# Kernel optimization log

Hardware: AMD Instinct MI355X
Metric: run time of the kernel (lower is better)

The kernel has to match this reference:

```python
import jax, jax.numpy as jnp
import numpy as np

B, T, C, HS = 8, 2048, 1024, 128

def setup_inputs() -> dict:
    key = jax.random.key(0)
    kx, kq, kk, kv = jax.random.split(key, 4)
    x = jax.random.normal(kx, (B, T, C), dtype=jnp.float32)
    # torch Linear(C, HS, bias=False): y = x @ W^T with W [HS, C].
    # We store the transposed form [C, HS] and right-multiply (same math).
    scale = 1.0 / np.sqrt(C)  # torch default init scale-ish; exact init irrelevant for correctness
    Wq = jax.random.normal(kq, (C, HS), dtype=jnp.float32) * scale
    Wk = jax.random.normal(kk, (C, HS), dtype=jnp.float32) * scale
    Wv = jax.random.normal(kv, (C, HS), dtype=jnp.float32) * scale
    return {"x": x, "Wq": Wq, "Wk": Wk, "Wv": Wv}

def reference(x, Wq, Wk, Wv):
    Bx, Tx, Cx = x.shape
    q = x @ Wq  # [B, T, HS]
    k = x @ Wk
    v = x @ Wv
    # NOTE: original scales by C**-0.5 where C = n_embd (not head_size)
    wei = jnp.einsum('btd,bsd->bts', q, k) * (Cx ** -0.5)  # [B, T, T]
    causal = jnp.tril(jnp.ones((Tx, Tx), dtype=bool))
    wei = jnp.where(causal, wei, -jnp.inf)
    wei = jax.nn.softmax(wei, axis=-1)
    # dropout rate 0.0 (eval semantics) -> identity
    return jnp.einsum('bts,bsd->btd', wei, v)  # [B, T, HS]
```

## Files before the change

kernel.cpp:

```cpp
#include <hip/hip_runtime.h>
#include <hip/hip_bf16.h>
#include <stdint.h>

typedef float f32x4 __attribute__((ext_vector_type(4)));
typedef float f32x4v __attribute__((ext_vector_type(4)));
typedef short short8 __attribute__((ext_vector_type(8)));
typedef unsigned short u16;
typedef unsigned short u16x8 __attribute__((ext_vector_type(8)));
typedef unsigned short u16x4 __attribute__((ext_vector_type(4)));

#define MFMA16x16x32 __builtin_amdgcn_mfma_f32_16x16x32_bf16

__device__ __forceinline__ u16 f2bf(float f) {
    unsigned int u = __builtin_bit_cast(unsigned int, f);
    u += 0x7fffu + ((u >> 16) & 1u);
    return (u16)(u >> 16);
}

__device__ __forceinline__ void gload_lds16(const void* g, void* l) {
    __builtin_amdgcn_global_load_lds(
        (const __attribute__((address_space(1))) uint32_t*)g,
        (__attribute__((address_space(3))) uint32_t*)l, 16, 0, 0);
}

__device__ __forceinline__ void barrier_lgkm() {
    asm volatile("s_waitcnt lgkmcnt(0)\n\ts_barrier" ::: "memory");
}

__global__ void k_transpose_wf(const float* __restrict__ Wq, const float* __restrict__ Wk,
                               const float* __restrict__ Wv, u16* __restrict__ WTf) {
    int tid  = blockIdx.x * 256 + threadIdx.x;
    int f    = tid >> 6;
    int lane = tid & 63;
    int kt  = f / 48;
    int rem = f % 48;
    int ks  = rem / 24;
    int nc  = rem % 24;
    int col = nc * 16 + (lane & 15);
    int w   = col >> 7, n = col & 127;
    int k0  = kt * 64 + ks * 32 + (lane >> 4) * 8;
    const float* W = (w == 0) ? Wq : ((w == 1) ? Wk : Wv);
    u16x8 v;
#pragma unroll
    for (int j = 0; j < 8; ++j)
        v[j] = f2bf(W[(size_t)(k0 + j) * 128 + n]);
    *(u16x8*)(&WTf[(size_t)tid * 8]) = v;
}

__global__ __launch_bounds__(256) void k_qkv_gemm5(
    const float* __restrict__ x, const u16* __restrict__ WTf,
    u16* __restrict__ qb, u16* __restrict__ kb, u16* __restrict__ vT)
{
    __shared__ u16 la[32 * 64];
    const int tid  = threadIdx.x;
    const int lane = tid & 63, wid = tid >> 6;
    const int lrow = lane & 15, lk = lane >> 4;
    const int m0 = blockIdx.x * 32;

    const int arow = tid >> 3;
    const int aseg = tid & 7;
    const float* xsrc = x + (size_t)(m0 + arow) * 1024 + aseg * 8;

    f32x4 acc[2][6];
#pragma unroll
    for (int i = 0; i < 2; ++i)
#pragma unroll
        for (int j = 0; j < 6; ++j) acc[i][j] = (f32x4){0.f, 0.f, 0.f, 0.f};

    f32x4v pa0 = *(const f32x4v*)xsrc;
    f32x4v pa1 = *(const f32x4v*)(xsrc + 4);

    for (int kt = 0; kt < 16; ++kt) {
        barrier_lgkm();
        {
            u16x8 v;
            v[0] = f2bf(pa0[0]); v[1] = f2bf(pa0[1]); v[2] = f2bf(pa0[2]); v[3] = f2bf(pa0[3]);
            v[4] = f2bf(pa1[0]); v[5] = f2bf(pa1[1]); v[6] = f2bf(pa1[2]); v[7] = f2bf(pa1[3]);
            *(u16x8*)(&la[arow * 64 + ((aseg ^ (arow & 7)) << 3)]) = v;
        }
        if (kt + 1 < 16) {
            pa0 = *(const f32x4v*)(xsrc + (kt + 1) * 64);
            pa1 = *(const f32x4v*)(xsrc + (kt + 1) * 64 + 4);
        }
        short8 bf[2][6];
#pragma unroll
        for (int ks = 0; ks < 2; ++ks)
#pragma unroll
            for (int nf = 0; nf < 6; ++nf)
                bf[ks][nf] = *(const short8*)(
                    WTf + ((size_t)((kt * 2 + ks) * 24 + wid * 6 + nf) * 64 + lane) * 8);
        barrier_lgkm();
#pragma unroll
        for (int ks = 0; ks < 2; ++ks) {
            short8 af[2];
#pragma unroll
            for (int mf = 0; mf < 2; ++mf) {
                int row = mf * 16 + lrow;
                int blk = (ks * 4 + lk) ^ (row & 7);
                af[mf] = *(const short8*)(&la[row * 64 + (blk << 3)]);
            }
#pragma unroll
            for (int mf = 0; mf < 2; ++mf)
#pragma unroll
                for (int nf = 0; nf < 6; ++nf)
                    acc[mf][nf] = MFMA16x16x32(af[mf], bf[ks][nf], acc[mf][nf], 0, 0, 0);
        }
    }

#pragma unroll
    for (int nf = 0; nf < 6; ++nf) {
        const int gc   = wid * 96 + nf * 16 + lrow;
        const int wsel = gc >> 7;
        const int col  = gc & 127;
#pragma unroll
        for (int mf = 0; mf < 2; ++mf) {
            const int row0 = m0 + mf * 16 + lk * 4;
            if (wsel == 0) {
#pragma unroll
                for (int jj = 0; jj < 4; ++jj)
                    qb[(size_t)(row0 + jj) * 128 + col] = f2bf(acc[mf][nf][jj]);
            } else if (wsel == 1) {
#pragma unroll
                for (int jj = 0; jj < 4; ++jj)
                    kb[(size_t)(row0 + jj) * 128 + col] = f2bf(acc[mf][nf][jj]);
            } else {
                const int bb = row0 >> 11, t0 = row0 & 2047;
                u16x4 v;
#pragma unroll
                for (int jj = 0; jj < 4; ++jj) v[jj] = f2bf(acc[mf][nf][jj]);
                *(u16x4*)(&vT[((size_t)bb * 128 + col) * 2048 + t0]) = v;
            }
        }
    }
}

__global__ __launch_bounds__(256) void k_flash5(
    const u16* __restrict__ qb, const u16* __restrict__ kb, const u16* __restrict__ vT,
    float* __restrict__ po, float* __restrict__ pm, float* __restrict__ pl)
{
    __shared__ u16 k_lds[64 * 128];
    __shared__ u16 v_lds[128 * 64];
    __shared__ u16 p_lds[4 * 16 * 64];
    const int tid  = threadIdx.x;
    const int lane = tid & 63, wid = tid >> 6;
    const int lrow = lane & 15, lk = lane >> 4;
    const int bx = blockIdx.x;
    const int b  = bx & 7;
    const int qt = (bx >> 3) & 31;
    const int z  = bx >> 8;

    const int nt   = qt + 1;
    const int base = (nt + 3) >> 2;
    const int t0   = z * base;
    const int t1   = (t0 + base < nt) ? (t0 + base) : nt;

    float* poslab = po + (size_t)bx * (64 * 128);
    if (t0 >= nt) {
        f32x4 zero = (f32x4){0.f, 0.f, 0.f, 0.f};
#pragma unroll
        for (int i = 0; i < 8; ++i)
            *(f32x4*)(&poslab[(tid + i * 256) * 4]) = zero;
        if (tid < 64) { pm[(size_t)bx * 64 + tid] = -1e30f; pl[(size_t)bx * 64 + tid] = 0.f; }
        return;
    }

    const int qrow0 = qt * 64;
    short8 qf[4];
    {
        const u16* qp = qb + ((size_t)b * 2048 + qrow0 + wid * 16 + lrow) * 128;
#pragma unroll
        for (int ks = 0; ks < 4; ++ks) qf[ks] = *(const short8*)(qp + ks * 32 + lk * 8);
    }
    f32x4 of[8];
#pragma unroll
    for (int i = 0; i < 8; ++i) of[i] = (f32x4){0.f, 0.f, 0.f, 0.f};
    float mrun[4], lsum[4];
#pragma unroll
    for (int j = 0; j < 4; ++j) { mrun[j] = -1e30f; lsum[j] = 0.f; }

    const u16* kbase = kb + (size_t)b * 2048 * 128;
    const u16* vbase = vT + (size_t)b * 128 * 2048;
    u16* pw = p_lds + wid * (16 * 64);

    for (int t = t0; t < t1; ++t) {
        const int kv0 = t << 6;
        __syncthreads();
#pragma unroll
        for (int i = 0; i < 4; ++i) {
            int c = tid + i * 256;
            int row = c >> 4, blk = c & 15;
            gload_lds16(kbase + (size_t)(kv0 + row) * 128 + ((blk ^ (row & 7)) << 3),
                        &k_lds[c * 8]);
        }
#pragma unroll
        for (int i = 0; i < 4; ++i) {
            int c = tid + i * 256;
            int row = c >> 3, blk = c & 7;
            gload_lds16(vbase + (size_t)row * 2048 + kv0 + ((blk ^ (row & 7)) << 3),
                        &v_lds[c * 8]);
        }
        __syncthreads();

        f32x4 sf[4];
#pragma unroll
        for (int nf = 0; nf < 4; ++nf) sf[nf] = (f32x4){0.f, 0.f, 0.f, 0.f};
#pragma unroll
        for (int ks = 0; ks < 4; ++ks)
#pragma unroll
            for (int nf = 0; nf < 4; ++nf) {
                int row = nf * 16 + lrow;
                int blk = (ks * 4 + lk) ^ (row & 7);
                short8 bfr = *(const short8*)(&k_lds[row * 128 + (blk << 3)]);
                sf[nf] = MFMA16x16x32(qf[ks], bfr, sf[nf], 0, 0, 0);
            }

        const bool diag = (t == qt);
#pragma unroll
        for (int nf = 0; nf < 4; ++nf)
#pragma unroll
            for (int jj = 0; jj < 4; ++jj) {
                float s = sf[nf][jj] * 0.03125f;
                if (diag && (nf * 16 + lrow > wid * 16 + lk * 4 + jj)) s = -1e30f;
                sf[nf][jj] = s;
            }
        float mt[4];
#pragma unroll
        for (int jj = 0; jj < 4; ++jj)
            mt[jj] = fmaxf(fmaxf(sf[0][jj], sf[1][jj]), fmaxf(sf[2][jj], sf[3][jj]));
#pragma unroll
        for (int off = 1; off < 16; off <<= 1)
#pragma unroll
            for (int jj = 0; jj < 4; ++jj)
                mt[jj] = fmaxf(mt[jj], __shfl_xor(mt[jj], off));
        bool small = true;
#pragma unroll
        for (int jj = 0; jj < 4; ++jj) small = small && (mt[jj] <= mrun[jj] + 8.f);
        if (!__all(small)) {
#pragma unroll
            for (int jj = 0; jj < 4; ++jj) {
                float mnew = fmaxf(mrun[jj], mt[jj]);
                float sc   = __expf(mrun[jj] - mnew);
                mrun[jj]   = mnew;
                lsum[jj]  *= sc;
#pragma unroll
                for (int df = 0; df < 8; ++df) of[df][jj] *= sc;
            }
        }
        float rs[4] = {0.f, 0.f, 0.f, 0.f};
#pragma unroll
        for (int nf = 0; nf < 4; ++nf)
#pragma unroll
            for (int jj = 0; jj < 4; ++jj) {
                float e = __expf(sf[nf][jj] - mrun[jj]);
                sf[nf][jj] = e;
                rs[jj] += e;
            }
#pragma unroll
        for (int off = 1; off < 16; off <<= 1)
#pragma unroll
            for (int jj = 0; jj < 4; ++jj)
                rs[jj] += __shfl_xor(rs[jj], off);
#pragma unroll
        for (int jj = 0; jj < 4; ++jj) lsum[jj] += rs[jj];

#pragma unroll
        for (int nf = 0; nf < 4; ++nf)
#pragma unroll
            for (int jj = 0; jj < 4; ++jj) {
                int row = lk * 4 + jj;
                int col = nf * 16 + lrow;
                pw[row * 64 + (((col >> 3) ^ (row & 7)) << 3) + (col & 7)] = f2bf(sf[nf][jj]);
            }
        asm volatile("s_waitcnt lgkmcnt(0)" ::: "memory");
        __builtin_amdgcn_sched_barrier(0);
        short8 paf[2];
#pragma unroll
        for (int ks2 = 0; ks2 < 2; ++ks2) {
            int blk = (ks2 * 4 + lk) ^ (lrow & 7);
            paf[ks2] = *(const short8*)(&pw[lrow * 64 + (blk << 3)]);
        }
#pragma unroll
        for (int ks2 = 0; ks2 < 2; ++ks2)
#pragma unroll
            for (int df = 0; df < 8; ++df) {
                int row = df * 16 + lrow;
                int blk = (ks2 * 4 + lk) ^ (row & 7);
                short8 vf = *(const short8*)(&v_lds[row * 64 + (blk << 3)]);
                of[df] = MFMA16x16x32(paf[ks2], vf, of[df], 0, 0, 0);
            }
    }

#pragma unroll
    for (int df = 0; df < 8; ++df)
#pragma unroll
        for (int jj = 0; jj < 4; ++jj)
            poslab[(size_t)(wid * 16 + lk * 4 + jj) * 128 + df * 16 + lrow] = of[df][jj];
    if (lrow == 0) {
#pragma unroll
        for (int jj = 0; jj < 4; ++jj) {
            pm[(size_t)bx * 64 + wid * 16 + lk * 4 + jj] = mrun[jj];
            pl[(size_t)bx * 64 + wid * 16 + lk * 4 + jj] = lsum[jj];
        }
    }
}

__global__ __launch_bounds__(256) void k_combine(
    const float* __restrict__ po, const float* __restrict__ pm, const float* __restrict__ pl,
    float* __restrict__ out)
{
    const int row  = blockIdx.x * 4 + (threadIdx.x >> 6);
    const int lane = threadIdx.x & 63;
    const int b  = row >> 11;
    const int t  = row & 2047;
    const int qt = t >> 6;
    const int r  = t & 63;

    float mz[4], lz[4];
#pragma unroll
    for (int z = 0; z < 4; ++z) {
        const size_t idx = (size_t)(b + 8 * qt + 256 * z) * 64 + r;
        mz[z] = pm[idx];
        lz[z] = pl[idx];
    }
    float M = fmaxf(fmaxf(mz[0], mz[1]), fmaxf(mz[2], mz[3]));
    float wz[4], den = 0.f;
#pragma unroll
    for (int z = 0; z < 4; ++z) { wz[z] = __expf(mz[z] - M); den += wz[z] * lz[z]; }
    float a0 = 0.f, a1 = 0.f;
#pragma unroll
    for (int z = 0; z < 4; ++z) {
        const float* slab = po + ((size_t)(b + 8 * qt + 256 * z) * 64 + r) * 128;
        a0 += wz[z] * slab[lane];
        a1 += wz[z] * slab[lane + 64];
    }
    float inv = 1.f / den;
    out[(size_t)row * 128 + lane]      = a0 * inv;
    out[(size_t)row * 128 + lane + 64] = a1 * inv;
}

extern "C" void kernel_launch(void* const* d_in, const int* in_sizes, int n_in,
                              void* d_out, int out_size, void* d_ws, size_t ws_size,
                              hipStream_t stream) {
    const float* x  = (const float*)d_in[0];
    const float* Wq = (const float*)d_in[1];
    const float* Wk = (const float*)d_in[2];
    const float* Wv = (const float*)d_in[3];
    float* out = (float*)d_out;

    char* ws = (char*)d_ws;
    u16*   qb  = (u16*)(ws);
    u16*   kb  = (u16*)(ws + (size_t)4  * 1048576);
    u16*   vT  = (u16*)(ws + (size_t)8  * 1048576);
    u16*   WTf = (u16*)(ws + (size_t)12 * 1048576);
    float* po  = (float*)(ws + (size_t)13 * 1048576);
    float* pm  = (float*)(ws + (size_t)47 * 1048576);
    float* pl  = (float*)(ws + (size_t)48 * 1048576);

    k_transpose_wf<<<192, 256, 0, stream>>>(Wq, Wk, Wv, WTf);
    k_qkv_gemm5<<<512, 256, 0, stream>>>(x, WTf, qb, kb, vT);
    k_flash5<<<1024, 256, 0, stream>>>(qb, kb, vT, po, pm, pl);
    k_combine<<<4096, 256, 0, stream>>>(po, pm, pl, out);
}
```

Baseline: 86.78 us.

## Pair causal query tiles for balanced split-KV work and double-buffer GEMM weights

The flash kernel no longer gives each query tile four fixed KV splits, a scheme that left many blocks empty and the rest uneven. It now pairs tile p with tile 31-p and spreads their combined 33 KV tiles over 8 blocks in proportion to each tile's length, so every block does about the same work. The combine kernel is updated to read only the splits that belong to each tile. Separately, the QKV GEMM double-buffers its weight fragments in registers so the next step's loads overlap the current MFMAs, which raises register pressure.

```diff
diff --git a/kernel.cpp b/kernel.cpp
--- a/kernel.cpp
+++ b/kernel.cpp
@@ -25,6 +25,11 @@
 
 __device__ __forceinline__ void barrier_lgkm() {
     asm volatile("s_waitcnt lgkmcnt(0)\n\ts_barrier" ::: "memory");
+}
+
+__device__ __forceinline__ int z_small(int na) {
+    int za = (8 * na + 32) / 33;
+    return za < 1 ? 1 : za;
 }
 
 __global__ void k_transpose_wf(const float* __restrict__ Wq, const float* __restrict__ Wk,
@@ -47,7 +52,7 @@
     *(u16x8*)(&WTf[(size_t)tid * 8]) = v;
 }
 
-__global__ __launch_bounds__(256) void k_qkv_gemm5(
+__global__ __launch_bounds__(256) void k_qkv_gemm6(
     const float* __restrict__ x, const u16* __restrict__ WTf,
     u16* __restrict__ qb, u16* __restrict__ kb, u16* __restrict__ vT)
 {
@@ -60,6 +65,7 @@
     const int arow = tid >> 3;
     const int aseg = tid & 7;
     const float* xsrc = x + (size_t)(m0 + arow) * 1024 + aseg * 8;
+    const u16* wb = WTf + (size_t)(wid * 6) * 512 + lane * 8;
 
     f32x4 acc[2][6];
 #pragma unroll
@@ -70,42 +76,52 @@
     f32x4v pa0 = *(const f32x4v*)xsrc;
     f32x4v pa1 = *(const f32x4v*)(xsrc + 4);
 
-    for (int kt = 0; kt < 16; ++kt) {
+#define LOADB(dst, ktv)                                                        \
+    _Pragma("unroll") for (int ks = 0; ks < 2; ++ks)                           \
+    _Pragma("unroll") for (int nf = 0; nf < 6; ++nf)                           \
+        dst[ks][nf] = *(const short8*)(wb + (size_t)(((ktv)*2 + ks)*24 + nf) * 512);
+
+#define STOREA()                                                               \
+    {   u16x8 v;                                                               \
+        v[0]=f2bf(pa0[0]); v[1]=f2bf(pa0[1]); v[2]=f2bf(pa0[2]); v[3]=f2bf(pa0[3]); \
+        v[4]=f2bf(pa1[0]); v[5]=f2bf(pa1[1]); v[6]=f2bf(pa1[2]); v[7]=f2bf(pa1[3]); \
+        *(u16x8*)(&la[arow * 64 + ((aseg ^ (arow & 7)) << 3)]) = v; }
+
+#define COMPUTE(bsrc)                                                          \
+    _Pragma("unroll") for (int ks = 0; ks < 2; ++ks) {                         \
+        short8 af[2];                                                          \
+        _Pragma("unroll") for (int mf = 0; mf < 2; ++mf) {                     \
+            int row = mf * 16 + lrow;                                          \
+            int blk = (ks * 4 + lk) ^ (row & 7);                               \
+            af[mf] = *(const short8*)(&la[row * 64 + (blk << 3)]);             \
+        }                                                                      \
+        _Pragma("unroll") for (int mf = 0; mf < 2; ++mf)                       \
+        _Pragma("unroll") for (int nf = 0; nf < 6; ++nf)                       \
+            acc[mf][nf] = MFMA16x16x32(af[mf], bsrc[ks][nf], acc[mf][nf], 0, 0, 0); }
+
+    short8 bA[2][6], bB[2][6];
+    LOADB(bA, 0);
+    for (int kt = 0; kt < 16; kt += 2) {
         barrier_lgkm();
-        {
-            u16x8 v;
-            v[0] = f2bf(pa0[0]); v[1] = f2bf(pa0[1]); v[2] = f2bf(pa0[2]); v[3] = f2bf(pa0[3]);
-            v[4] = f2bf(pa1[0]); v[5] = f2bf(pa1[1]); v[6] = f2bf(pa1[2]); v[7] = f2bf(pa1[3]);
-            *(u16x8*)(&la[arow * 64 + ((aseg ^ (arow & 7)) << 3)]) = v;
-        }
-        if (kt + 1 < 16) {
-            pa0 = *(const f32x4v*)(xsrc + (kt + 1) * 64);
-            pa1 = *(const f32x4v*)(xsrc + (kt + 1) * 64 + 4);
-        }
-        short8 bf[2][6];
-#pragma unroll
-        for (int ks = 0; ks < 2; ++ks)
-#pragma unroll
-            for (int nf = 0; nf < 6; ++nf)
-                bf[ks][nf] = *(const short8*)(
-                    WTf + ((size_t)((kt * 2 + ks) * 24 + wid * 6 + nf) * 64 + lane) * 8);
+        STOREA();
+        pa0 = *(const f32x4v*)(xsrc + (kt + 1) * 64);
+        pa1 = *(const f32x4v*)(xsrc + (kt + 1) * 64 + 4);
+        LOADB(bB, kt + 1);
         barrier_lgkm();
-#pragma unroll
-        for (int ks = 0; ks < 2; ++ks) {
-            short8 af[2];
-#pragma unroll
-            for (int mf = 0; mf < 2; ++mf) {
-                int row = mf * 16 + lrow;
-                int blk = (ks * 4 + lk) ^ (row & 7);
-                af[mf] = *(const short8*)(&la[row * 64 + (blk << 3)]);
-            }
-#pragma unroll
-            for (int mf = 0; mf < 2; ++mf)
-#pragma unroll
-                for (int nf = 0; nf < 6; ++nf)
-                    acc[mf][nf] = MFMA16x16x32(af[mf], bf[ks][nf], acc[mf][nf], 0, 0, 0);
-        }
-    }
+        COMPUTE(bA);
+        barrier_lgkm();
+        STOREA();
+        if (kt + 2 < 16) {
+            pa0 = *(const f32x4v*)(xsrc + (kt + 2) * 64);
+            pa1 = *(const f32x4v*)(xsrc + (kt + 2) * 64 + 4);
+            LOADB(bA, kt + 2);
+        }
+        barrier_lgkm();
+        COMPUTE(bB);
+    }
+#undef LOADB
+#undef STOREA
+#undef COMPUTE
 
 #pragma unroll
     for (int nf = 0; nf < 6; ++nf) {
@@ -134,7 +150,7 @@
     }
 }
 
-__global__ __launch_bounds__(256) void k_flash5(
+__global__ __launch_bounds__(256) void k_flash6(
     const u16* __restrict__ qb, const u16* __restrict__ kb, const u16* __restrict__ vT,
     float* __restrict__ po, float* __restrict__ pm, float* __restrict__ pl)
 {
@@ -146,23 +162,16 @@
     const int lrow = lane & 15, lk = lane >> 4;
     const int bx = blockIdx.x;
     const int b  = bx & 7;
-    const int qt = (bx >> 3) & 31;
-    const int z  = bx >> 8;
-
-    const int nt   = qt + 1;
-    const int base = (nt + 3) >> 2;
-    const int t0   = z * base;
-    const int t1   = (t0 + base < nt) ? (t0 + base) : nt;
-
-    float* poslab = po + (size_t)bx * (64 * 128);
-    if (t0 >= nt) {
-        f32x4 zero = (f32x4){0.f, 0.f, 0.f, 0.f};
-#pragma unroll
-        for (int i = 0; i < 8; ++i)
-            *(f32x4*)(&poslab[(tid + i * 256) * 4]) = zero;
-        if (tid < 64) { pm[(size_t)bx * 64 + tid] = -1e30f; pl[(size_t)bx * 64 + tid] = 0.f; }
-        return;
-    }
+    const int p  = (bx >> 3) & 15;
+    const int z  = bx >> 7;
+
+    const int na = p + 1;
+    const int za = z_small(na);
+    int qt, n, k, Z;
+    if (z < za) { qt = p;      n = na;     k = z;      Z = za;     }
+    else        { qt = 31 - p; n = 32 - p; k = z - za; Z = 8 - za; }
+    const int t0 = (k * n) / Z;
+    const int t1 = ((k + 1) * n) / Z;
 
     const int qrow0 = qt * 64;
     short8 qf[4];
@@ -214,7 +223,7 @@
                 sf[nf] = MFMA16x16x32(qf[ks], bfr, sf[nf], 0, 0, 0);
             }
 
-        const bool diag = (t == qt);
+        const bool diag = (t == n - 1);
 #pragma unroll
         for (int nf = 0; nf < 4; ++nf)
 #pragma unroll
@@ -290,6 +299,7 @@
             }
     }
 
+    float* poslab = po + (size_t)bx * (64 * 128);
 #pragma unroll
     for (int df = 0; df < 8; ++df)
 #pragma unroll
@@ -315,25 +325,24 @@
     const int qt = t >> 6;
     const int r  = t & 63;
 
-    float mz[4], lz[4];
-#pragma unroll
-    for (int z = 0; z < 4; ++z) {
-        const size_t idx = (size_t)(b + 8 * qt + 256 * z) * 64 + r;
-        mz[z] = pm[idx];
-        lz[z] = pl[idx];
-    }
-    float M = fmaxf(fmaxf(mz[0], mz[1]), fmaxf(mz[2], mz[3]));
-    float wz[4], den = 0.f;
-#pragma unroll
-    for (int z = 0; z < 4; ++z) { wz[z] = __expf(mz[z] - M); den += wz[z] * lz[z]; }
-    float a0 = 0.f, a1 = 0.f;
-#pragma unroll
-    for (int z = 0; z < 4; ++z) {
-        const float* slab = po + ((size_t)(b + 8 * qt + 256 * z) * 64 + r) * 128;
-        a0 += wz[z] * slab[lane];
-        a1 += wz[z] * slab[lane + 64];
-    }
-    float inv = 1.f / den;
+    const int p  = (qt < 16) ? qt : 31 - qt;
+    const int za = z_small(p + 1);
+    const int zlo = (qt < 16) ? 0 : za;
+    const int zhi = (qt < 16) ? za : 8;
+
+    float M = -1e30f;
+    for (int z = zlo; z < zhi; ++z)
+        M = fmaxf(M, pm[(size_t)(b + 8 * p + 128 * z) * 64 + r]);
+    float den = 0.f, a0 = 0.f, a1 = 0.f;
+    for (int z = zlo; z < zhi; ++z) {
+        const int bxp = b + 8 * p + 128 * z;
+        const float w = __expf(pm[(size_t)bxp * 64 + r] - M);
+        den += w * pl[(size_t)bxp * 64 + r];
+        const float* slab = po + ((size_t)bxp * 64 + r) * 128;
+        a0 += w * slab[lane];
+        a1 += w * slab[lane + 64];
+    }
+    const float inv = 1.f / den;
     out[(size_t)row * 128 + lane]      = a0 * inv;
     out[(size_t)row * 128 + lane + 64] = a1 * inv;
 }
@@ -357,7 +366,7 @@
     float* pl  = (float*)(ws + (size_t)48 * 1048576);
 
     k_transpose_wf<<<192, 256, 0, stream>>>(Wq, Wk, Wv, WTf);
-    k_qkv_gemm5<<<512, 256, 0, stream>>>(x, WTf, qb, kb, vT);
-    k_flash5<<<1024, 256, 0, stream>>>(qb, kb, vT, po, pm, pl);
+    k_qkv_gemm6<<<512, 256, 0, stream>>>(x, WTf, qb, kb, vT);
+    k_flash6<<<1024, 256, 0, stream>>>(qb, kb, vT, po, pm, pl);
     k_combine<<<4096, 256, 0, stream>>>(po, pm, pl, out);
 }
```

New measurement: 80.24 us. 1.08x faster.
